# Kernel optimization log

Measured on AMD Instinct MI355X. Metric: run time of the kernel, lower is better.

Reference implementation:

```python
import jax, jax.numpy as jnp
import numpy as np

B, CIN, C, N, K = 2, 64, 128, 8192, 16
GROUPS = C // 16
EPS = 1e-5


def lrelu(x):
    return jnp.where(x >= 0, x, 0.1 * x)


def conv1d(x, w, b):  # x:(B,Ci,N) w:(Co,Ci)
    return jnp.einsum('oc,bcn->bon', w, x) + b[None, :, None]


def conv2d(x, w, b):  # x:(B,Ci,N,K) w:(Co,Ci)
    return jnp.einsum('oc,bcnk->bonk', w, x) + b[None, :, None, None]


def groupnorm(x, gamma, beta, groups=GROUPS):
    # normalize over (C/groups, *spatial) per sample per group
    b, c = x.shape[0], x.shape[1]
    xr = x.reshape(b, groups, -1)
    mean = xr.mean(-1, keepdims=True)
    var = xr.var(-1, keepdims=True)
    xn = ((xr - mean) * jax.lax.rsqrt(var + EPS)).reshape(x.shape)
    shp = (1, c) + (1,) * (x.ndim - 2)
    return xn * gamma.reshape(shp) + beta.reshape(shp)


def knn_idx(xyz, k):  # xyz:(B,3,N) -> idx:(B,N,K)
    pts = jnp.transpose(xyz, (0, 2, 1))  # (B,N,3)
    sq = jnp.sum(pts * pts, axis=-1)  # (B,N)
    inner = jnp.einsum('bnc,bmc->bnm', pts, pts)
    d2 = sq[:, :, None] + sq[:, None, :] - 2.0 * inner  # (B,N,N)
    _, idx = jax.lax.top_k(-d2, k)
    return idx


def group(x, idx):  # x:(B,C,N) idx:(B,N,K) -> (B,C,N,K)
    b, c, n = x.shape
    k = idx.shape[-1]
    idxe = jnp.broadcast_to(idx.reshape(b, 1, n * k), (b, c, n * k))
    return jnp.take_along_axis(x, idxe, axis=2).reshape(b, c, n, k)


def reference(xyz, feat, pre_w, pre_b, wq_w, wq_b, wk_w, wk_b, wv_w, wv_b,
              pos1_w, pos1_b, pos1_g, pos1_be, pos2_w, pos2_b,
              att1_w, att1_b, att1_g, att1_be, att2_w, att2_b,
              post_w, post_b, post_g, post_be):
    idx = knn_idx(xyz, K)  # (B,N,K)
    new_feat = conv1d(feat, pre_w, pre_b)  # (B,C,N)
    rel = group(xyz, idx) - xyz[:, :, :, None]  # (B,3,N,K)
    pos = lrelu(groupnorm(conv2d(rel, pos1_w, pos1_b), pos1_g, pos1_be))
    pos = conv2d(pos, pos2_w, pos2_b)  # (B,C,N,K)
    q = conv1d(new_feat, wq_w, wq_b)
    k = group(conv1d(new_feat, wk_w, wk_b), idx)  # (B,C,N,K)
    v = group(conv1d(new_feat, wv_w, wv_b), idx)
    att = q[:, :, :, None] - k + pos
    att = lrelu(groupnorm(conv2d(att, att1_w, att1_b), att1_g, att1_be))
    att = conv2d(att, att2_w, att2_b)
    att = jax.nn.softmax(att, axis=3)
    out = jnp.sum(att * v, axis=3)  # (B,C,N)
    out = lrelu(groupnorm(conv1d(out + new_feat, post_w, post_b), post_g, post_be))
    return out


def setup_inputs():
    key = jax.random.key(0)
    ks = jax.random.split(key, 16)
    s = 0.05
    d = {
        'xyz': jax.random.normal(ks[0], (B, 3, N), jnp.float32),
        'feat': jax.random.normal(ks[1], (B, CIN, N), jnp.float32),
        'pre_w': jax.random.normal(ks[2], (C, CIN), jnp.float32) * s,
        'pre_b': jnp.zeros((C,), jnp.float32),
        'wq_w': jax.random.normal(ks[3], (C, C), jnp.float32) * s,
        'wq_b': jnp.zeros((C,), jnp.float32),
        'wk_w': jax.random.normal(ks[4], (C, C), jnp.float32) * s,
        'wk_b': jnp.zeros((C,), jnp.float32),
        'wv_w': jax.random.normal(ks[5], (C, C), jnp.float32) * s,
        'wv_b': jnp.zeros((C,), jnp.float32),
        'pos1_w': jax.random.normal(ks[6], (C, 3), jnp.float32) * s,
        'pos1_b': jnp.zeros((C,), jnp.float32),
        'pos1_g': jnp.ones((C,), jnp.float32),
        'pos1_be': jnp.zeros((C,), jnp.float32),
        'pos2_w': jax.random.normal(ks[7], (C, C), jnp.float32) * s,
        'pos2_b': jnp.zeros((C,), jnp.float32),
        'att1_w': jax.random.normal(ks[8], (C, C), jnp.float32) * s,
        'att1_b': jnp.zeros((C,), jnp.float32),
        'att1_g': jnp.ones((C,), jnp.float32),
        'att1_be': jnp.zeros((C,), jnp.float32),
        'att2_w': jax.random.normal(ks[9], (C, C), jnp.float32) * s,
        'att2_b': jnp.zeros((C,), jnp.float32),
        'post_w': jax.random.normal(ks[10], (C, C), jnp.float32) * s,
        'post_b': jnp.zeros((C,), jnp.float32),
        'post_g': jnp.ones((C,), jnp.float32),
        'post_be': jnp.zeros((C,), jnp.float32),
    }
    return d
```

## Files before the change

kernel.cpp:

```cpp
#include <hip/hip_runtime.h>
#include <hip/hip_bf16.h>

#define BB 2
#define NN 8192
#define CC 128
#define CIN_ 64
#define KK 16
#define EPSV 1e-5f

typedef __attribute__((ext_vector_type(8))) short short8;
typedef __attribute__((ext_vector_type(4))) float f32x4;

static const size_t OFF_NF   = 262144;
static const size_t OFF_OUT2 = OFF_NF  + 2097152;
static const size_t OFF_Y    = OFF_OUT2 + 2097152;
static const size_t OFF_AQB  = OFF_Y   + 16777216;
static const size_t OFF_AKB  = OFF_AQB + 1048576;
static const size_t OFF_VFB  = OFF_AKB + 1048576;
static const size_t OFF_WQ2  = OFF_VFB + 1048576;
static const size_t OFF_WK2  = OFF_WQ2 + 16384;
static const size_t OFF_PWT  = OFF_WK2 + 16384;
static const size_t OFF_W2B  = OFF_PWT + 16384;
static const size_t OFF_A2B  = OFF_W2B + 8192;
static const size_t OFF_BY   = OFF_A2B + 8192;
static const size_t OFF_RST  = OFF_BY  + 128;
static const size_t OFF_REDA = OFF_RST + 32;
static const size_t OFF_REDP = OFF_REDA + 32;
static const size_t OFF_S1   = OFF_REDP + 32;
static const size_t OFF_T1   = OFF_S1 + 256;
static const size_t OFF_S2   = OFF_T1 + 256;
static const size_t OFF_T2   = OFF_S2 + 256;
static const size_t OFF_S3   = OFF_T2 + 256;
static const size_t OFF_T3   = OFF_S3 + 256;
static const size_t OFF_PTS4 = OFF_T3 + 256;
static const size_t OFF_PTA  = OFF_PTS4 + 65536;
static const size_t OFF_PTP  = OFF_PTA + 65536;

__device__ __forceinline__ unsigned fkey_u(float d) {
  unsigned u = __float_as_uint(d);
  return (u & 0x80000000u) ? ~u : (u | 0x80000000u);
}
__device__ __forceinline__ unsigned long long shflx64(unsigned long long v, int m) {
  int lo = __shfl_xor((int)(unsigned)(v & 0xffffffffu), m, 64);
  int hi = __shfl_xor((int)(unsigned)(v >> 32), m, 64);
  return ((unsigned long long)(unsigned)hi << 32) | (unsigned)lo;
}
__device__ __forceinline__ float bf2f(unsigned short u) {
  return __uint_as_float((unsigned)u << 16);
}
__device__ __forceinline__ unsigned short f2bf(float f) {
  __hip_bfloat16 h = __float2bfloat16(f);
  unsigned short r;
  __builtin_memcpy(&r, &h, 2);
  return r;
}
__device__ __forceinline__ unsigned pack2bf(float a, float b) {
  return (unsigned)f2bf(a) | ((unsigned)f2bf(b) << 16);
}

__global__ __launch_bounds__(128) void prep_weights(
    const float* __restrict__ att1_w, const float* __restrict__ wq_w, const float* __restrict__ wk_w,
    const float* __restrict__ pos2_w, const float* __restrict__ att2_w, const float* __restrict__ post_w,
    const float* __restrict__ wq_b, const float* __restrict__ wk_b, const float* __restrict__ pos2_b,
    const float* __restrict__ att1_b,
    float* __restrict__ WQ2, float* __restrict__ WK2, __hip_bfloat16* __restrict__ W2b,
    __hip_bfloat16* __restrict__ A2b, float* __restrict__ PWT, float* __restrict__ bias_y) {
  int blk = blockIdx.x, t = threadIdx.x;
  if (blk < 128) {
    int c = blk;
    __shared__ float row[128];
    row[t] = att1_w[c * 128 + t];
    __syncthreads();
    float sq = 0.f, sk = 0.f, sp = 0.f;
    for (int m = 0; m < 128; ++m) {
      float r = row[m];
      sq = fmaf(r, wq_w[m * 128 + t], sq);
      sk = fmaf(r, wk_w[m * 128 + t], sk);
      sp = fmaf(r, pos2_w[m * 128 + t], sp);
    }
    WQ2[c * 128 + t] = sq;
    WK2[c * 128 + t] = sk;
    W2b[c * 128 + t] = __float2bfloat16(sp);
  } else if (blk == 128) {
    for (int e = t; e < 16384; e += 128) {
      int c = e >> 7, cp = e & 127;
      A2b[e] = __float2bfloat16(att2_w[e]);
      PWT[cp * 128 + c] = post_w[e];
    }
  } else {
    float s = att1_b[t];
    for (int m = 0; m < 128; ++m)
      s = fmaf(att1_w[t * 128 + m], wq_b[m] - wk_b[m] + pos2_b[m], s);
    bias_y[t] = s;
  }
}

__global__ __launch_bounds__(256) void pts4_kernel(const float* __restrict__ xyz,
                                                   float4* __restrict__ pts4) {
  int e = blockIdx.x * 256 + threadIdx.x;
  int b = e >> 13, n = e & 8191;
  const float* X = xyz + b * 3 * NN;
  float x = X[n], y = X[NN + n], z = X[2 * NN + n];
  pts4[e] = make_float4(-2.0f * x, -2.0f * y, -2.0f * z, fmaf(z, z, fmaf(y, y, x * x)));
}

#define SLOTS 96
__global__ __launch_bounds__(256) void knn_kernel(const float4* __restrict__ pts4,
                                                  int* __restrict__ idxb) {
  __shared__ unsigned long long list[16][SLOTS];
  __shared__ float chm[16][33];
  __shared__ float taus[16];
  __shared__ int cnt[16];
  int t = threadIdx.x;
  int wid = t >> 6, lane = t & 63;
  int blk = blockIdx.x;
  int b = blk >> 9;
  int q0 = (blk & 511) << 4;
  const float4* P = pts4 + b * NN;
  if (t < 16) cnt[t] = 0;
  float qx[16], qy[16], qz[16];
#pragma unroll
  for (int j = 0; j < 16; ++j) {
    float4 qv = P[q0 + j];
    qx[j] = -0.5f * qv.x; qy[j] = -0.5f * qv.y; qz[j] = -0.5f * qv.z;
  }

  {
    int g = lane >> 3, s = lane & 7;
    const float4* Pc = P + (wid << 11) + (g << 8);
    float mn[16];
#pragma unroll
    for (int j = 0; j < 16; ++j) mn[j] = 3.4e38f;
    for (int i = 0; i < 32; i += 2) {
      float4 c0 = Pc[(i << 3) + s];
      float4 c1 = Pc[((i + 1) << 3) + s];
#pragma unroll
      for (int j = 0; j < 16; ++j) {
        float d0 = fmaf(qx[j], c0.x, fmaf(qy[j], c0.y, fmaf(qz[j], c0.z, c0.w)));
        float d1 = fmaf(qx[j], c1.x, fmaf(qy[j], c1.y, fmaf(qz[j], c1.z, c1.w)));
        mn[j] = fminf(mn[j], fminf(d0, d1));
      }
    }
#pragma unroll
    for (int off = 1; off < 8; off <<= 1)
#pragma unroll
      for (int j = 0; j < 16; ++j) mn[j] = fminf(mn[j], __shfl_xor(mn[j], off));
    if (s == 0) {
#pragma unroll
      for (int j = 0; j < 16; ++j) chm[j][(wid << 3) + g] = mn[j];
    }
  }
  __syncthreads();

  if (t < 16) {
    float v[32];
#pragma unroll
    for (int i = 0; i < 32; ++i) v[i] = chm[t][i];
    float lo = v[0], hi = v[0];
#pragma unroll
    for (int i = 1; i < 32; ++i) { lo = fminf(lo, v[i]); hi = fmaxf(hi, v[i]); }
    for (int it = 0; it < 12; ++it) {
      float mid = 0.5f * (lo + hi);
      int c = 0;
#pragma unroll
      for (int i = 0; i < 32; ++i) c += (v[i] <= mid) ? 1 : 0;
      if (c >= 16) hi = mid; else lo = mid;
    }
    taus[t] = hi;
  }
  __syncthreads();
  float tauv[16];
#pragma unroll
  for (int j = 0; j < 16; ++j) tauv[j] = taus[j];

  for (int i = 0; i < 32; ++i) {
    int ci = (wid << 11) + (i << 6) + lane;
    float4 cv = P[ci];
#pragma unroll
    for (int j = 0; j < 16; ++j) {
      float d = fmaf(qx[j], cv.x, fmaf(qy[j], cv.y, fmaf(qz[j], cv.z, cv.w)));
      if (d <= tauv[j]) {
        int sl = atomicAdd(&cnt[j], 1);
        if (sl < SLOTS)
          list[j][sl] = ((unsigned long long)fkey_u(d) << 32) | (unsigned)ci;
      }
    }
  }
  __syncthreads();

  for (int pp = 0; pp < 2; ++pp) {
    int qa = (wid << 2) + pp * 2, qb2 = qa + 1;
    int ca = cnt[qa]; if (ca > SLOTS) ca = SLOTS;
    int cb3 = cnt[qb2]; if (cb3 > SLOTS) cb3 = SLOTS;
    unsigned long long k0a = (lane < ca) ? list[qa][lane] : ~0ULL;
    unsigned long long k1a = (lane + 64 < ca) ? list[qa][lane + 64] : ~0ULL;
    unsigned long long k0b = (lane < cb3) ? list[qb2][lane] : ~0ULL;
    unsigned long long k1b = (lane + 64 < cb3) ? list[qb2][lane + 64] : ~0ULL;
    for (int r = 0; r < 16; ++r) {
      unsigned long long wa = (k0a < k1a) ? k0a : k1a;
      unsigned long long wb = (k0b < k1b) ? k0b : k1b;
      for (int off = 32; off; off >>= 1) {
        unsigned long long oa = shflx64(wa, off);
        unsigned long long ob = shflx64(wb, off);
        if (oa < wa) wa = oa;
        if (ob < wb) wb = ob;
      }
      if (k0a == wa) k0a = ~0ULL; else if (k1a == wa) k1a = ~0ULL;
      if (k0b == wb) k0b = ~0ULL; else if (k1b == wb) k1b = ~0ULL;
      if (lane == 0) {
        idxb[((size_t)(b * NN) + q0 + qa) * 16 + r] = (int)(wa & 0xffffffffu);
        idxb[((size_t)(b * NN) + q0 + qb2) * 16 + r] = (int)(wb & 0xffffffffu);
      }
    }
  }
}

__global__ __launch_bounds__(256) void relstats_kernel(const float* __restrict__ xyz,
                                                       const int* __restrict__ idxb,
                                                       float* __restrict__ rst) {
  int b = blockIdx.x >> 8;
  int nbase = (blockIdx.x & 255) << 5;
  const float* X = xyz + b * 3 * NN;
  float a[9];
#pragma unroll
  for (int m = 0; m < 9; ++m) a[m] = 0.f;
  for (int e = threadIdx.x; e < 512; e += 256) {
    int nn = nbase + (e >> 4);
    int kk = e & 15;
    int j = idxb[(b * NN + nn) * 16 + kk];
    float rx = X[j] - X[nn];
    float ry = X[NN + j] - X[NN + nn];
    float rz = X[2 * NN + j] - X[2 * NN + nn];
    a[0] += rx; a[1] += ry; a[2] += rz;
    a[3] = fmaf(rx, rx, a[3]); a[4] = fmaf(rx, ry, a[4]); a[5] = fmaf(rx, rz, a[5]);
    a[6] = fmaf(ry, ry, a[6]); a[7] = fmaf(ry, rz, a[7]); a[8] = fmaf(rz, rz, a[8]);
  }
  __shared__ float red[4][9];
  int lane = threadIdx.x & 63, wid = threadIdx.x >> 6;
#pragma unroll
  for (int m = 0; m < 9; ++m) {
    float v = a[m];
    for (int off = 32; off; off >>= 1) v += __shfl_xor(v, off, 64);
    if (lane == 0) red[wid][m] = v;
  }
  __syncthreads();
  if (threadIdx.x < 9) {
    float v = red[0][threadIdx.x] + red[1][threadIdx.x] + red[2][threadIdx.x] + red[3][threadIdx.x];
    atomicAdd(&rst[b * 16 + threadIdx.x], v);
  }
}

__global__ __launch_bounds__(256) void t1_kernel(const float* __restrict__ rst,
    const float* __restrict__ pos1_w, const float* __restrict__ pos1_b,
    const float* __restrict__ pos1_g, const float* __restrict__ pos1_be,
    float* __restrict__ s1, float* __restrict__ t1) {
  __shared__ float gsum[16], gsum2[16];
  int t = threadIdx.x;
  if (t < 16) { gsum[t] = 0.f; gsum2[t] = 0.f; }
  __syncthreads();
  int b = t >> 7, c = t & 127;
  const float* S = rst + b * 16;
  const float Minv = 1.0f / (float)(NN * KK);
  float mx = S[0] * Minv, my = S[1] * Minv, mz = S[2] * Minv;
  float Mxx = S[3] * Minv, Mxy = S[4] * Minv, Mxz = S[5] * Minv;
  float Myy = S[6] * Minv, Myz = S[7] * Minv, Mzz = S[8] * Minv;
  float w0 = pos1_w[c * 3], w1 = pos1_w[c * 3 + 1], w2 = pos1_w[c * 3 + 2];
  float bb = pos1_b[c];
  float wm = w0 * mx + w1 * my + w2 * mz;
  float Ey = wm + bb;
  float q = w0 * w0 * Mxx + w1 * w1 * Myy + w2 * w2 * Mzz
          + 2.f * (w0 * w1 * Mxy + w0 * w2 * Mxz + w1 * w2 * Myz);
  float Ey2 = q + 2.f * bb * wm + bb * bb;
  int g = c >> 4;
  atomicAdd(&gsum[b * 8 + g], Ey);
  atomicAdd(&gsum2[b * 8 + g], Ey2);
  __syncthreads();
  float mean = gsum[b * 8 + g] * (1.f / 16.f);
  float var = fmaxf(gsum2[b * 8 + g] * (1.f / 16.f) - mean * mean, 0.f);
  float r = rsqrtf(var + EPSV);
  float sv = pos1_g[c] * r;
  s1[t] = sv;
  t1[t] = fmaf(sv, bb, pos1_be[c] - mean * sv);
}

__global__ __launch_bounds__(256) void feat_kernel(
    const float* __restrict__ feat, const float* __restrict__ pre_w, const float* __restrict__ pre_b,
    const float* __restrict__ WQ2, const float* __restrict__ WK2,
    const float* __restrict__ wv_w, const float* __restrict__ wv_b,
    float* __restrict__ nf, __hip_bfloat16* __restrict__ AqTb,
    __hip_bfloat16* __restrict__ AkTb, __hip_bfloat16* __restrict__ vfTb) {
  int b = blockIdx.x >> 9;
  int n0 = (blockIdx.x & 511) << 4;
  __shared__ float fe[64][20];
  __shared__ float nfs[128][20];
  int t = threadIdx.x;
  for (int e = t; e < 1024; e += 256) {
    int ci = e >> 4, nn2 = e & 15;
    fe[ci][nn2] = feat[(b * 64 + ci) * NN + n0 + nn2];
  }
  __syncthreads();
  int nq = t & 3, cw = t >> 2;
  {
    float acc[2][4];
#pragma unroll
    for (int m = 0; m < 2; ++m) {
      float bv = pre_b[cw + 64 * m];
      acc[m][0] = bv; acc[m][1] = bv; acc[m][2] = bv; acc[m][3] = bv;
    }
    for (int i = 0; i < 64; ++i) {
      float4 x = *(const float4*)&fe[i][nq << 2];
      float w0 = pre_w[cw * 64 + i];
      float w1 = pre_w[(cw + 64) * 64 + i];
      acc[0][0] = fmaf(w0, x.x, acc[0][0]); acc[0][1] = fmaf(w0, x.y, acc[0][1]);
      acc[0][2] = fmaf(w0, x.z, acc[0][2]); acc[0][3] = fmaf(w0, x.w, acc[0][3]);
      acc[1][0] = fmaf(w1, x.x, acc[1][0]); acc[1][1] = fmaf(w1, x.y, acc[1][1]);
      acc[1][2] = fmaf(w1, x.z, acc[1][2]); acc[1][3] = fmaf(w1, x.w, acc[1][3]);
    }
#pragma unroll
    for (int m = 0; m < 2; ++m) {
      int c = cw + 64 * m;
      float4 v = make_float4(acc[m][0], acc[m][1], acc[m][2], acc[m][3]);
      *(float4*)&nfs[c][nq << 2] = v;
      *(float4*)&nf[(b * 128 + c) * NN + n0 + (nq << 2)] = v;
    }
  }
  __syncthreads();
  for (int s = 0; s < 3; ++s) {
    const float* Wm = (s == 0) ? WQ2 : ((s == 1) ? WK2 : wv_w);
    __hip_bfloat16* D = (s == 0) ? AqTb : ((s == 1) ? AkTb : vfTb);
    float acc[2][4];
#pragma unroll
    for (int m = 0; m < 2; ++m) {
      float bv = (s == 2) ? wv_b[cw + 64 * m] : 0.f;
      acc[m][0] = bv; acc[m][1] = bv; acc[m][2] = bv; acc[m][3] = bv;
    }
    for (int i = 0; i < 128; ++i) {
      float4 x = *(const float4*)&nfs[i][nq << 2];
      float w0 = Wm[cw * 128 + i];
      float w1 = Wm[(cw + 64) * 128 + i];
      acc[0][0] = fmaf(w0, x.x, acc[0][0]); acc[0][1] = fmaf(w0, x.y, acc[0][1]);
      acc[0][2] = fmaf(w0, x.z, acc[0][2]); acc[0][3] = fmaf(w0, x.w, acc[0][3]);
      acc[1][0] = fmaf(w1, x.x, acc[1][0]); acc[1][1] = fmaf(w1, x.y, acc[1][1]);
      acc[1][2] = fmaf(w1, x.z, acc[1][2]); acc[1][3] = fmaf(w1, x.w, acc[1][3]);
    }
#pragma unroll
    for (int m = 0; m < 2; ++m) {
      int c = cw + 64 * m;
#pragma unroll
      for (int v = 0; v < 4; ++v)
        D[(size_t)(b * NN + n0 + (nq << 2) + v) * 128 + c] = __float2bfloat16(acc[m][v]);
    }
  }
}

__global__ __launch_bounds__(256) void y_kernel_mfma(const float* __restrict__ xyz,
    const int* __restrict__ idxb, const __hip_bfloat16* __restrict__ AqTb,
    const __hip_bfloat16* __restrict__ AkTb, const __hip_bfloat16* __restrict__ W2b,
    const float* __restrict__ bias_y, const float* __restrict__ pos1_w,
    const float* __restrict__ s1, const float* __restrict__ t1,
    __hip_bfloat16* __restrict__ ybuf, float* __restrict__ partA) {
  int b = blockIdx.x >> 11;
  int pb = (blockIdx.x & 2047) * 4;
  __shared__ __align__(16) __hip_bfloat16 z_s[64][136];
  __shared__ __align__(16) __hip_bfloat16 ak_s[64][136];
  __shared__ __align__(16) float aq_s[4][128];
  __shared__ float rel_s[64][4];
  __shared__ int jj[64];
  __shared__ float gns[8], gns2[8];
  int t = threadIdx.x;
  int lane = t & 63, wid = t >> 6;
  int l15 = lane & 15, quad = lane >> 4;
  if (t < 8) { gns[t] = 0.f; gns2[t] = 0.f; }
  if (t < 64) {
    int n = pb + (t >> 4);
    int j = idxb[(b * NN + pb) * 16 + t];
    jj[t] = j;
    const float* X = xyz + b * 3 * NN;
    rel_s[t][0] = X[j] - X[n];
    rel_s[t][1] = X[NN + j] - X[NN + n];
    rel_s[t][2] = X[2 * NN + j] - X[2 * NN + n];
  }
  for (int e = t; e < 512; e += 256) {
    int pt = e >> 7, c = e & 127;
    aq_s[pt][c] = bf2f(((const unsigned short*)AqTb)[((size_t)(b * NN) + pb + pt) * 128 + c]) + bias_y[c];
  }
  __syncthreads();
  {
    int cpp = t & 63, pg = t >> 6;
    int cp0 = cpp * 2;
    float w00 = pos1_w[cp0 * 3], w01 = pos1_w[cp0 * 3 + 1], w02 = pos1_w[cp0 * 3 + 2];
    float w10 = pos1_w[cp0 * 3 + 3], w11 = pos1_w[cp0 * 3 + 4], w12 = pos1_w[cp0 * 3 + 5];
    float sa = s1[b * 128 + cp0], ta = t1[b * 128 + cp0];
    float sb = s1[b * 128 + cp0 + 1], tb = t1[b * 128 + cp0 + 1];
#pragma unroll
    for (int i = 0; i < 16; ++i) {
      int pix = pg * 16 + i;
      float rx = rel_s[pix][0], ry = rel_s[pix][1], rz = rel_s[pix][2];
      float u0 = fmaf(w02, rz, fmaf(w01, ry, w00 * rx));
      float u1 = fmaf(w12, rz, fmaf(w11, ry, w10 * rx));
      float z0 = fmaf(sa, u0, ta); z0 = (z0 >= 0.f) ? z0 : 0.1f * z0;
      float z1 = fmaf(sb, u1, tb); z1 = (z1 >= 0.f) ? z1 : 0.1f * z1;
      *(unsigned*)&z_s[pix][cp0] = pack2bf(z0, z1);
    }
  }
  for (int e = t; e < 4096; e += 256) {
    int pix = e >> 6, cpp = e & 63;
    *(unsigned*)&ak_s[pix][cpp * 2] =
        *(const unsigned*)((const unsigned short*)AkTb + ((size_t)(b * NN) + jj[pix]) * 128 + cpp * 2);
  }
  short8 afr[2][4];
#pragma unroll
  for (int m2 = 0; m2 < 2; ++m2) {
    int row = (wid * 2 + m2) * 16 + l15;
#pragma unroll
    for (int k0 = 0; k0 < 4; ++k0)
      afr[m2][k0] = *(const short8*)((const unsigned short*)W2b + row * 128 + k0 * 32 + quad * 8);
  }
  __syncthreads();
  f32x4 acc[2][4];
#pragma unroll
  for (int m2 = 0; m2 < 2; ++m2)
#pragma unroll
    for (int nt = 0; nt < 4; ++nt) acc[m2][nt] = (f32x4){0.f, 0.f, 0.f, 0.f};
#pragma unroll
  for (int k0 = 0; k0 < 4; ++k0) {
#pragma unroll
    for (int nt = 0; nt < 4; ++nt) {
      short8 bfr = *(const short8*)&z_s[nt * 16 + l15][k0 * 32 + quad * 8];
      acc[0][nt] = __builtin_amdgcn_mfma_f32_16x16x32_bf16(afr[0][k0], bfr, acc[0][nt], 0, 0, 0);
      acc[1][nt] = __builtin_amdgcn_mfma_f32_16x16x32_bf16(afr[1][k0], bfr, acc[1][nt], 0, 0, 0);
    }
  }
  float lsum[2] = {0.f, 0.f}, lsum2[2] = {0.f, 0.f};
#pragma unroll
  for (int m2 = 0; m2 < 2; ++m2) {
    int c0 = (wid * 2 + m2) * 16 + quad * 4;
#pragma unroll
    for (int nt = 0; nt < 4; ++nt) {
      int pix = nt * 16 + l15;
      ushort4 au = *(ushort4*)&ak_s[pix][c0];
      float4 aq = *(float4*)&aq_s[nt][c0];
      f32x4 a = acc[m2][nt];
      float v0 = a[0] + aq.x - bf2f(au.x);
      float v1 = a[1] + aq.y - bf2f(au.y);
      float v2 = a[2] + aq.z - bf2f(au.z);
      float v3 = a[3] + aq.w - bf2f(au.w);
      lsum[m2] += (v0 + v1) + (v2 + v3);
      lsum2[m2] += fmaf(v0, v0, fmaf(v1, v1, fmaf(v2, v2, v3 * v3)));
      ushort4 yo;
      yo.x = f2bf(v0); yo.y = f2bf(v1); yo.z = f2bf(v2); yo.w = f2bf(v3);
      *(ushort4*)&ak_s[pix][c0] = yo;
    }
  }
#pragma unroll
  for (int m2 = 0; m2 < 2; ++m2) {
    float s = lsum[m2], s2 = lsum2[m2];
    for (int msk = 1; msk < 64; msk <<= 1) {
      s += __shfl_xor(s, msk);
      s2 += __shfl_xor(s2, msk);
    }
    if (lane == 0) {
      atomicAdd(&gns[wid * 2 + m2], s);
      atomicAdd(&gns2[wid * 2 + m2], s2);
    }
  }
  __syncthreads();
  size_t ybase = ((size_t)(b * NN) + pb) * 16;
  unsigned short* yb = (unsigned short*)ybuf;
  for (int e = t; e < 4096; e += 256) {
    int pix = e >> 6, cpp = e & 63;
    *(unsigned*)(yb + (ybase + pix) * 128 + cpp * 2) = *(unsigned*)&ak_s[pix][cpp * 2];
  }
  if (t < 8) {
    partA[(size_t)t * 4096 + blockIdx.x] = gns[t];
    partA[(size_t)(8 + t) * 4096 + blockIdx.x] = gns2[t];
  }
}

__global__ __launch_bounds__(256) void gnred_kernel(const float* __restrict__ part,
                                                    float* __restrict__ red) {
  int k = blockIdx.x;
  int pb = k >> 4, idx = k & 15;
  const float* p = part + (size_t)idx * 4096 + pb * 2048;
  float s = 0.f;
  for (int i = threadIdx.x; i < 2048; i += 256) s += p[i];
  __shared__ float rs[4];
  int lane = threadIdx.x & 63, wid = threadIdx.x >> 6;
  for (int off = 32; off; off >>= 1) s += __shfl_xor(s, off);
  if (lane == 0) rs[wid] = s;
  __syncthreads();
  if (threadIdx.x == 0) red[k] = rs[0] + rs[1] + rs[2] + rs[3];
}

__global__ __launch_bounds__(256) void gnaff_kernel(const float* __restrict__ red,
    const float* __restrict__ gamma, const float* __restrict__ beta, float Minv,
    float* __restrict__ sarr, float* __restrict__ tarr) {
  int t = threadIdx.x;
  int b = t >> 7, c = t & 127, g = c >> 4;
  float S = red[b * 16 + g], S2 = red[b * 16 + 8 + g];
  float mean = S * Minv;
  float var = fmaxf(S2 * Minv - mean * mean, 0.f);
  float r = rsqrtf(var + EPSV);
  float sv = gamma[c] * r;
  sarr[t] = sv;
  tarr[t] = beta[c] - mean * sv;
}

__global__ __launch_bounds__(256) void att_out_kernel(const __hip_bfloat16* __restrict__ ybuf,
    const int* __restrict__ idxb, const float* __restrict__ s2, const float* __restrict__ t2,
    const __hip_bfloat16* __restrict__ A2b, const __hip_bfloat16* __restrict__ vfTb,
    const float* __restrict__ nf, const float* __restrict__ PWT, const float* __restrict__ post_b,
    float* __restrict__ out2, float* __restrict__ partP) {
  int b = blockIdx.x >> 11;
  int pb = (blockIdx.x & 2047) * 4;
  __shared__ __align__(16) union HS {
    unsigned short h[64][136];
    float sc[2][128][17];
  } hs;
  __shared__ __align__(16) __hip_bfloat16 v_s[64][136];
  __shared__ __align__(16) float opre[4][132];
  __shared__ int jj[64];
  __shared__ float gns[8], gns2[8];
  int t = threadIdx.x;
  int lane = t & 63, wid = t >> 6;
  int l15 = lane & 15, quad = lane >> 4;
  if (t < 8) { gns[t] = 0.f; gns2[t] = 0.f; }
  if (t < 64) jj[t] = idxb[(b * NN + pb) * 16 + t];
  __syncthreads();
  size_t ybase = ((size_t)(b * NN) + pb) * 16;
  const unsigned short* yb = (const unsigned short*)ybuf;
  {
    int cpp = t & 63, pg = t >> 6;
    int c0 = cpp * 2;
    float sa = s2[b * 128 + c0], ta = t2[b * 128 + c0];
    float sb = s2[b * 128 + c0 + 1], tb = t2[b * 128 + c0 + 1];
#pragma unroll
    for (int i = 0; i < 16; ++i) {
      int pix = pg * 16 + i;
      unsigned u = *(const unsigned*)(yb + (ybase + pix) * 128 + c0);
      float y0 = bf2f((unsigned short)(u & 0xffff));
      float y1 = bf2f((unsigned short)(u >> 16));
      float h0 = fmaf(sa, y0, ta); h0 = (h0 >= 0.f) ? h0 : 0.1f * h0;
      float h1 = fmaf(sb, y1, tb); h1 = (h1 >= 0.f) ? h1 : 0.1f * h1;
      *(unsigned*)&hs.h[pix][c0] = pack2bf(h0, h1);
    }
  }
  for (int e = t; e < 4096; e += 256) {
    int pix = e >> 6, cpp = e & 63;
    *(unsigned*)&v_s[pix][cpp * 2] =
        *(const unsigned*)((const unsigned short*)vfTb + ((size_t)(b * NN) + jj[pix]) * 128 + cpp * 2);
  }
  short8 afr[2][4];
#pragma unroll
  for (int m2 = 0; m2 < 2; ++m2) {
    int row = (wid * 2 + m2) * 16 + l15;
#pragma unroll
    for (int k0 = 0; k0 < 4; ++k0)
      afr[m2][k0] = *(const short8*)((const unsigned short*)A2b + row * 128 + k0 * 32 + quad * 8);
  }
  __syncthreads();
  f32x4 acc[2][4];
#pragma unroll
  for (int m2 = 0; m2 < 2; ++m2)
#pragma unroll
    for (int nt = 0; nt < 4; ++nt) acc[m2][nt] = (f32x4){0.f, 0.f, 0.f, 0.f};
#pragma unroll
  for (int k0 = 0; k0 < 4; ++k0) {
#pragma unroll
    for (int nt = 0; nt < 4; ++nt) {
      short8 bfr = *(const short8*)&hs.h[nt * 16 + l15][k0 * 32 + quad * 8];
      acc[0][nt] = __builtin_amdgcn_mfma_f32_16x16x32_bf16(afr[0][k0], bfr, acc[0][nt], 0, 0, 0);
      acc[1][nt] = __builtin_amdgcn_mfma_f32_16x16x32_bf16(afr[1][k0], bfr, acc[1][nt], 0, 0, 0);
    }
  }
  int pidx = t >> 7;
  int cch = t & 127;
#pragma unroll
  for (int pass = 0; pass < 2; ++pass) {
    __syncthreads();
#pragma unroll
    for (int ntl = 0; ntl < 2; ++ntl) {
      int nt = pass * 2 + ntl;
#pragma unroll
      for (int m2 = 0; m2 < 2; ++m2) {
        int cb = (wid * 2 + m2) * 16 + quad * 4;
        f32x4 a = acc[m2][nt];
#pragma unroll
        for (int r = 0; r < 4; ++r) hs.sc[ntl][cb + r][l15] = a[r];
      }
    }
    __syncthreads();
    {
      int p = pass * 2 + pidx;
      float nfv = nf[(size_t)(b * 128 + cch) * NN + pb + p];
      const float* srow = hs.sc[pidx][cch];
      float sv[16];
#pragma unroll
      for (int k = 0; k < 16; ++k) sv[k] = srow[k];
      float mx = sv[0];
#pragma unroll
      for (int k = 1; k < 16; ++k) mx = fmaxf(mx, sv[k]);
      float sm = 0.f, dot = 0.f;
#pragma unroll
      for (int k = 0; k < 16; ++k) {
        float e = __expf(sv[k] - mx);
        sm += e;
        float vv = bf2f(*(const unsigned short*)&v_s[p * 16 + k][cch]);
        dot = fmaf(e, vv, dot);
      }
      opre[p][cch] = dot / sm + nfv;
    }
  }
  __syncthreads();
  {
    int c = t & 127, g = t >> 7;
    float a0 = post_b[c], a1 = a0;
    for (int cp = 0; cp < 128; ++cp) {
      float w = PWT[cp * 128 + c];
      a0 = fmaf(w, opre[g * 2][cp], a0);
      a1 = fmaf(w, opre[g * 2 + 1][cp], a1);
    }
    out2[(size_t)(b * 128 + c) * NN + pb + g * 2] = a0;
    out2[(size_t)(b * 128 + c) * NN + pb + g * 2 + 1] = a1;
    atomicAdd(&gns[c >> 4], a0 + a1);
    atomicAdd(&gns2[c >> 4], fmaf(a0, a0, a1 * a1));
  }
  __syncthreads();
  if (t < 8) {
    partP[(size_t)t * 4096 + blockIdx.x] = gns[t];
    partP[(size_t)(8 + t) * 4096 + blockIdx.x] = gns2[t];
  }
}

__global__ __launch_bounds__(256) void final_kernel(const float* __restrict__ out2,
    const float* __restrict__ s3, const float* __restrict__ t3, float* __restrict__ out) {
  int e = blockIdx.x * 256 + threadIdx.x;
  int c = (e >> 13) & 127, b = e >> 20;
  float v = fmaf(s3[b * 128 + c], out2[e], t3[b * 128 + c]);
  out[e] = (v >= 0.f) ? v : 0.1f * v;
}

extern "C" void kernel_launch(void* const* d_in, const int* in_sizes, int n_in,
                              void* d_out, int out_size, void* d_ws, size_t ws_size,
                              hipStream_t stream) {
  (void)in_sizes; (void)n_in; (void)out_size; (void)ws_size;
  const float* xyz     = (const float*)d_in[0];
  const float* feat    = (const float*)d_in[1];
  const float* pre_w   = (const float*)d_in[2];
  const float* pre_b   = (const float*)d_in[3];
  const float* wq_w    = (const float*)d_in[4];
  const float* wq_b    = (const float*)d_in[5];
  const float* wk_w    = (const float*)d_in[6];
  const float* wk_b    = (const float*)d_in[7];
  const float* wv_w    = (const float*)d_in[8];
  const float* wv_b    = (const float*)d_in[9];
  const float* pos1_w  = (const float*)d_in[10];
  const float* pos1_b  = (const float*)d_in[11];
  const float* pos1_g  = (const float*)d_in[12];
  const float* pos1_be = (const float*)d_in[13];
  const float* pos2_w  = (const float*)d_in[14];
  const float* pos2_b  = (const float*)d_in[15];
  const float* att1_w  = (const float*)d_in[16];
  const float* att1_b  = (const float*)d_in[17];
  const float* att1_g  = (const float*)d_in[18];
  const float* att1_be = (const float*)d_in[19];
  const float* att2_w  = (const float*)d_in[20];
  const float* post_w  = (const float*)d_in[22];
  const float* post_b  = (const float*)d_in[23];
  const float* post_g  = (const float*)d_in[24];
  const float* post_be = (const float*)d_in[25];

  float* W = (float*)d_ws;
  int* idxb = (int*)d_ws;
  float* nf   = W + OFF_NF;
  float* out2 = W + OFF_OUT2;
  __hip_bfloat16* ybuf = (__hip_bfloat16*)(W + OFF_Y);
  __hip_bfloat16* AqTb = (__hip_bfloat16*)(W + OFF_AQB);
  __hip_bfloat16* AkTb = (__hip_bfloat16*)(W + OFF_AKB);
  __hip_bfloat16* vfTb = (__hip_bfloat16*)(W + OFF_VFB);
  float* WQ2  = W + OFF_WQ2;
  float* WK2  = W + OFF_WK2;
  float* PWT  = W + OFF_PWT;
  __hip_bfloat16* W2b = (__hip_bfloat16*)(W + OFF_W2B);
  __hip_bfloat16* A2b = (__hip_bfloat16*)(W + OFF_A2B);
  float* BY   = W + OFF_BY;
  float* RST  = W + OFF_RST;
  float* REDA = W + OFF_REDA;
  float* REDP = W + OFF_REDP;
  float* S1 = W + OFF_S1; float* T1 = W + OFF_T1;
  float* S2 = W + OFF_S2; float* T2 = W + OFF_T2;
  float* S3 = W + OFF_S3; float* T3 = W + OFF_T3;
  float4* PTS4 = (float4*)(W + OFF_PTS4);
  float* PARTA = W + OFF_PTA;
  float* PARTP = W + OFF_PTP;

  hipMemsetAsync(RST, 0, 32 * sizeof(float), stream);

  prep_weights<<<130, 128, 0, stream>>>(att1_w, wq_w, wk_w, pos2_w, att2_w, post_w,
                                        wq_b, wk_b, pos2_b, att1_b,
                                        WQ2, WK2, W2b, A2b, PWT, BY);
  pts4_kernel<<<64, 256, 0, stream>>>(xyz, PTS4);
  knn_kernel<<<1024, 256, 0, stream>>>(PTS4, idxb);
  relstats_kernel<<<512, 256, 0, stream>>>(xyz, idxb, RST);
  t1_kernel<<<1, 256, 0, stream>>>(RST, pos1_w, pos1_b, pos1_g, pos1_be, S1, T1);
  feat_kernel<<<1024, 256, 0, stream>>>(feat, pre_w, pre_b, WQ2, WK2, wv_w, wv_b,
                                        nf, AqTb, AkTb, vfTb);
  y_kernel_mfma<<<4096, 256, 0, stream>>>(xyz, idxb, AqTb, AkTb, W2b, BY, pos1_w, S1, T1, ybuf, PARTA);
  gnred_kernel<<<32, 256, 0, stream>>>(PARTA, REDA);
  gnaff_kernel<<<1, 256, 0, stream>>>(REDA, att1_g, att1_be, 1.0f / 2097152.0f, S2, T2);
  att_out_kernel<<<4096, 256, 0, stream>>>(ybuf, idxb, S2, T2, A2b, vfTb, nf, PWT, post_b, out2, PARTP);
  gnred_kernel<<<32, 256, 0, stream>>>(PARTP, REDP);
  gnaff_kernel<<<1, 256, 0, stream>>>(REDP, post_g, post_be, 1.0f / 131072.0f, S3, T3);
  final_kernel<<<8192, 256, 0, stream>>>(out2, S3, T3, (float*)d_out);
}
```

Measured before the change: 378.3 us.

## Widen kNN blocks to 512 threads and fold GroupNorm affine into consumers

The kNN kernel now launches 512 threads per block, so each wave covers half as many candidates in the chunk-min pass, the tau-filter pass and the final selection, which raises parallelism per query tile. Separately, the two single-block gnaff launches are removed, and the GroupNorm scale and shift are recomputed inline in att_out_kernel and final_kernel from the reduced sums. This cuts launch overhead and serialization between stages, at the cost of a few redundant rsqrt and loads per thread. The 512-thread kNN block also needs more registers per block, which could reduce occupancy.

Measured after the change: 383.0 us. Within noise of the previous version (+1.3%).

```diff
diff --git a/kernel.cpp b/kernel.cpp
--- a/kernel.cpp
+++ b/kernel.cpp
@@ -105,7 +105,7 @@
 }
 
 #define SLOTS 96
-__global__ __launch_bounds__(256) void knn_kernel(const float4* __restrict__ pts4,
+__global__ __launch_bounds__(512) void knn_kernel(const float4* __restrict__ pts4,
                                                   int* __restrict__ idxb) {
   __shared__ unsigned long long list[16][SLOTS];
   __shared__ float chm[16][33];
@@ -126,14 +126,14 @@
   }
 
   {
-    int g = lane >> 3, s = lane & 7;
-    const float4* Pc = P + (wid << 11) + (g << 8);
+    int g = lane >> 4, s = lane & 15;
+    const float4* Pc = P + (wid << 10) + (g << 8);
     float mn[16];
 #pragma unroll
     for (int j = 0; j < 16; ++j) mn[j] = 3.4e38f;
-    for (int i = 0; i < 32; i += 2) {
-      float4 c0 = Pc[(i << 3) + s];
-      float4 c1 = Pc[((i + 1) << 3) + s];
+    for (int i = 0; i < 16; i += 2) {
+      float4 c0 = Pc[(i << 4) + s];
+      float4 c1 = Pc[((i + 1) << 4) + s];
 #pragma unroll
       for (int j = 0; j < 16; ++j) {
         float d0 = fmaf(qx[j], c0.x, fmaf(qy[j], c0.y, fmaf(qz[j], c0.z, c0.w)));
@@ -142,12 +142,12 @@
       }
     }
 #pragma unroll
-    for (int off = 1; off < 8; off <<= 1)
+    for (int off = 1; off < 16; off <<= 1)
 #pragma unroll
       for (int j = 0; j < 16; ++j) mn[j] = fminf(mn[j], __shfl_xor(mn[j], off));
     if (s == 0) {
 #pragma unroll
-      for (int j = 0; j < 16; ++j) chm[j][(wid << 3) + g] = mn[j];
+      for (int j = 0; j < 16; ++j) chm[j][(wid << 2) + g] = mn[j];
     }
   }
   __syncthreads();
@@ -173,8 +173,8 @@
 #pragma unroll
   for (int j = 0; j < 16; ++j) tauv[j] = taus[j];
 
-  for (int i = 0; i < 32; ++i) {
-    int ci = (wid << 11) + (i << 6) + lane;
+  for (int i = 0; i < 16; ++i) {
+    int ci = (wid << 10) + (i << 6) + lane;
     float4 cv = P[ci];
 #pragma unroll
     for (int j = 0; j < 16; ++j) {
@@ -188,8 +188,8 @@
   }
   __syncthreads();
 
-  for (int pp = 0; pp < 2; ++pp) {
-    int qa = (wid << 2) + pp * 2, qb2 = qa + 1;
+  {
+    int qa = wid << 1, qb2 = qa + 1;
     int ca = cnt[qa]; if (ca > SLOTS) ca = SLOTS;
     int cb3 = cnt[qb2]; if (cb3 > SLOTS) cb3 = SLOTS;
     unsigned long long k0a = (lane < ca) ? list[qa][lane] : ~0ULL;
@@ -492,22 +492,9 @@
   if (threadIdx.x == 0) red[k] = rs[0] + rs[1] + rs[2] + rs[3];
 }
 
-__global__ __launch_bounds__(256) void gnaff_kernel(const float* __restrict__ red,
-    const float* __restrict__ gamma, const float* __restrict__ beta, float Minv,
-    float* __restrict__ sarr, float* __restrict__ tarr) {
-  int t = threadIdx.x;
-  int b = t >> 7, c = t & 127, g = c >> 4;
-  float S = red[b * 16 + g], S2 = red[b * 16 + 8 + g];
-  float mean = S * Minv;
-  float var = fmaxf(S2 * Minv - mean * mean, 0.f);
-  float r = rsqrtf(var + EPSV);
-  float sv = gamma[c] * r;
-  sarr[t] = sv;
-  tarr[t] = beta[c] - mean * sv;
-}
-
 __global__ __launch_bounds__(256) void att_out_kernel(const __hip_bfloat16* __restrict__ ybuf,
-    const int* __restrict__ idxb, const float* __restrict__ s2, const float* __restrict__ t2,
+    const int* __restrict__ idxb, const float* __restrict__ redA,
+    const float* __restrict__ att1_g, const float* __restrict__ att1_be,
     const __hip_bfloat16* __restrict__ A2b, const __hip_bfloat16* __restrict__ vfTb,
     const float* __restrict__ nf, const float* __restrict__ PWT, const float* __restrict__ post_b,
     float* __restrict__ out2, float* __restrict__ partP) {
@@ -532,8 +519,16 @@
   {
     int cpp = t & 63, pg = t >> 6;
     int c0 = cpp * 2;
-    float sa = s2[b * 128 + c0], ta = t2[b * 128 + c0];
-    float sb = s2[b * 128 + c0 + 1], tb = t2[b * 128 + c0 + 1];
+    const float Minv = 1.0f / 2097152.0f;
+    int g = c0 >> 4;
+    float S = redA[b * 16 + g], S2v = redA[b * 16 + 8 + g];
+    float mean = S * Minv;
+    float var = fmaxf(S2v * Minv - mean * mean, 0.f);
+    float r = rsqrtf(var + EPSV);
+    float sa = att1_g[c0] * r;
+    float ta = att1_be[c0] - mean * sa;
+    float sb = att1_g[c0 + 1] * r;
+    float tb = att1_be[c0 + 1] - mean * sb;
 #pragma unroll
     for (int i = 0; i < 16; ++i) {
       int pix = pg * 16 + i;
@@ -633,10 +628,19 @@
 }
 
 __global__ __launch_bounds__(256) void final_kernel(const float* __restrict__ out2,
-    const float* __restrict__ s3, const float* __restrict__ t3, float* __restrict__ out) {
+    const float* __restrict__ redP, const float* __restrict__ post_g,
+    const float* __restrict__ post_be, float* __restrict__ out) {
   int e = blockIdx.x * 256 + threadIdx.x;
   int c = (e >> 13) & 127, b = e >> 20;
-  float v = fmaf(s3[b * 128 + c], out2[e], t3[b * 128 + c]);
+  const float Minv = 1.0f / 131072.0f;
+  int g = c >> 4;
+  float S = redP[b * 16 + g], S2 = redP[b * 16 + 8 + g];
+  float mean = S * Minv;
+  float var = fmaxf(S2 * Minv - mean * mean, 0.f);
+  float r = rsqrtf(var + EPSV);
+  float sv = post_g[c] * r;
+  float tv = post_be[c] - mean * sv;
+  float v = fmaf(sv, out2[e], tv);
   out[e] = (v >= 0.f) ? v : 0.1f * v;
 }
 
@@ -688,8 +692,6 @@
   float* REDA = W + OFF_REDA;
   float* REDP = W + OFF_REDP;
   float* S1 = W + OFF_S1; float* T1 = W + OFF_T1;
-  float* S2 = W + OFF_S2; float* T2 = W + OFF_T2;
-  float* S3 = W + OFF_S3; float* T3 = W + OFF_T3;
   float4* PTS4 = (float4*)(W + OFF_PTS4);
   float* PARTA = W + OFF_PTA;
   float* PARTP = W + OFF_PTP;
@@ -700,16 +702,15 @@
                                         wq_b, wk_b, pos2_b, att1_b,
                                         WQ2, WK2, W2b, A2b, PWT, BY);
   pts4_kernel<<<64, 256, 0, stream>>>(xyz, PTS4);
-  knn_kernel<<<1024, 256, 0, stream>>>(PTS4, idxb);
+  knn_kernel<<<1024, 512, 0, stream>>>(PTS4, idxb);
   relstats_kernel<<<512, 256, 0, stream>>>(xyz, idxb, RST);
   t1_kernel<<<1, 256, 0, stream>>>(RST, pos1_w, pos1_b, pos1_g, pos1_be, S1, T1);
   feat_kernel<<<1024, 256, 0, stream>>>(feat, pre_w, pre_b, WQ2, WK2, wv_w, wv_b,
                                         nf, AqTb, AkTb, vfTb);
   y_kernel_mfma<<<4096, 256, 0, stream>>>(xyz, idxb, AqTb, AkTb, W2b, BY, pos1_w, S1, T1, ybuf, PARTA);
   gnred_kernel<<<32, 256, 0, stream>>>(PARTA, REDA);
-  gnaff_kernel<<<1, 256, 0, stream>>>(REDA, att1_g, att1_be, 1.0f / 2097152.0f, S2, T2);
-  att_out_kernel<<<4096, 256, 0, stream>>>(ybuf, idxb, S2, T2, A2b, vfTb, nf, PWT, post_b, out2, PARTP);
+  att_out_kernel<<<4096, 256, 0, stream>>>(ybuf, idxb, REDA, att1_g, att1_be,
+                                           A2b, vfTb, nf, PWT, post_b, out2, PARTP);
   gnred_kernel<<<32, 256, 0, stream>>>(PARTP, REDP);
-  gnaff_kernel<<<1, 256, 0, stream>>>(REDP, post_g, post_be, 1.0f / 131072.0f, S3, T3);
-  final_kernel<<<8192, 256, 0, stream>>>(out2, S3, T3, (float*)d_out);
-}
+  final_kernel<<<8192, 256, 0, stream>>>(out2, REDP, post_g, post_be, (float*)d_out);
+}
```
